# Kernel tuning notes

Measured on AMD Instinct MI355X. Metric: run time of the kernel, lower is better.

Reference implementation:

```python
import jax, jax.numpy as jnp
import numpy as np

B, T, I, H, O = 64, 512, 256, 1024, 10

def setup_inputs() -> dict:
    key = jax.random.key(0)
    ks = jax.random.split(key, 7)
    s_x = 1.0 / np.sqrt(I)
    s_h = 1.0 / np.sqrt(H)
    return {
        "x": jax.random.normal(ks[0], (B, T, I), dtype=jnp.float32),
        "Wx": jax.random.uniform(ks[1], (4, I, H), jnp.float32, -s_x, s_x),
        "bx": jax.random.uniform(ks[2], (4, H), jnp.float32, -s_x, s_x),
        "Wh": jax.random.uniform(ks[3], (4, H, H), jnp.float32, -s_h, s_h),
        "bh": jax.random.uniform(ks[4], (4, H), jnp.float32, -s_h, s_h),
        "Wp": jax.random.uniform(ks[5], (H, O), jnp.float32, -s_h, s_h),
        "bp": jax.random.uniform(ks[6], (O,), jnp.float32, -s_h, s_h),
    }

def reference(x, Wx, bx, Wh, bh, Wp, bp):
    # Gate order along axis 0: g (tanh), i, f, o (sigmoid).
    batch, seq, _ = x.shape
    hid = Wh.shape[-1]
    # Precompute all input-side gate projections: [T, 4, B, H]
    gx_all = jnp.einsum('bti,kih->tkbh', x, Wx) + bx[None, :, None, :]

    def step(carry, gx_t):
        h, c = carry
        z = gx_t + jnp.einsum('bh,kho->kbo', h, Wh) + bh[:, None, :]  # [4,B,H]
        g = jnp.tanh(z[0])
        i = jax.nn.sigmoid(z[1])
        f = jax.nn.sigmoid(z[2])
        o = jax.nn.sigmoid(z[3])
        c = g * i + c * f
        h = jnp.tanh(c) * o
        return (h, c), None

    h0 = jnp.zeros((batch, hid), dtype=x.dtype)
    c0 = jnp.zeros((batch, hid), dtype=x.dtype)
    (h, _), _ = jax.lax.scan(step, (h0, c0), gx_all)
    p = h @ Wp + bp
    return jax.nn.softmax(p, axis=1)
```

## Files before the change

### kernel.cpp

```cpp
#include <hip/hip_runtime.h>
#include <cstdint>
#include <cstddef>

#define B_  64
#define T_  512
#define I_  256
#define H_  1024
#define O_  10
#define ZST 68
#define ZPW (64 * ZST)
#define ZBUF (4 * ZPW)
#define LDS_ALLOC 139264

typedef __attribute__((ext_vector_type(4))) float f32x4;
typedef __attribute__((ext_vector_type(8))) short s16x8;
typedef unsigned long long u64;

__device__ inline unsigned short f2bf(float f) {
    unsigned int u = __float_as_uint(f);
    u += 0x7fffu + ((u >> 16) & 1u);
    return (unsigned short)(u >> 16);
}
__device__ inline float bf2f(unsigned short h) {
    return __uint_as_float(((unsigned int)h) << 16);
}
__device__ inline float fsig(float x)  { return 1.0f / (1.0f + __expf(-x)); }
__device__ inline float ftanh(float x) { return 1.0f - 2.0f / (1.0f + __expf(2.0f * x)); }

#define ALD32(p)    __hip_atomic_load((p), __ATOMIC_RELAXED, __HIP_MEMORY_SCOPE_AGENT)
#define AST32(p, v) __hip_atomic_store((p), (v), __ATOMIC_RELAXED, __HIP_MEMORY_SCOPE_AGENT)
#define ALD64(p)    __hip_atomic_load((p), __ATOMIC_RELAXED, __HIP_MEMORY_SCOPE_AGENT)
#define AST64(p, v) __hip_atomic_store((p), (v), __ATOMIC_RELAXED, __HIP_MEMORY_SCOPE_AGENT)

__global__ __launch_bounds__(256) void cast_xT_kernel(const float* __restrict__ x,
                                                      unsigned short* __restrict__ xb) {
    int idx = blockIdx.x * 256 + threadIdx.x;
    int ic4 = idx & 63, rest = idx >> 6;
    int t = rest & 511, b = rest >> 9;
    float4 v = ((const float4*)x)[((size_t)(b * T_ + t)) * 64 + ic4];
    ((ushort4*)xb)[((size_t)(t * B_ + b)) * 64 + ic4] =
        make_ushort4(f2bf(v.x), f2bf(v.y), f2bf(v.z), f2bf(v.w));
}

__global__ __launch_bounds__(256) void pack_wh_kernel(const float* __restrict__ Wh,
                                                      uint4* __restrict__ whp) {
    int e = blockIdx.x * 256 + threadIdx.x;
    int lane = e & 63, nt = (e >> 6) & 3, kt = (e >> 8) & 31, nb = e >> 13;
    int q = (lane & 15) >> 2, cc = lane & 3;
    int hh = nb * 16 + nt * 4 + cc;
    int k0 = kt * 32 + (lane >> 4) * 8;
    const float* src = Wh + (size_t)q * (H_ * H_) + (size_t)k0 * H_ + hh;
    unsigned short u[8];
#pragma unroll
    for (int j = 0; j < 8; ++j) u[j] = f2bf(src[(size_t)j * H_]);
    uint4 out;
    out.x = (unsigned)u[0] | ((unsigned)u[1] << 16);
    out.y = (unsigned)u[2] | ((unsigned)u[3] << 16);
    out.z = (unsigned)u[4] | ((unsigned)u[5] << 16);
    out.w = (unsigned)u[6] | ((unsigned)u[7] << 16);
    whp[e] = out;
}

__global__ __launch_bounds__(256) void pack_wx_kernel(const float* __restrict__ Wx,
                                                      uint4* __restrict__ wxp) {
    int e = blockIdx.x * 256 + threadIdx.x;
    int lane = e & 63, nt = (e >> 6) & 3, kt = (e >> 8) & 7, nb = e >> 11;
    int q = (lane & 15) >> 2, cc = lane & 3;
    int hh = nb * 16 + nt * 4 + cc;
    int i0 = kt * 32 + (lane >> 4) * 8;
    const float* src = Wx + (size_t)q * (I_ * H_) + (size_t)i0 * H_ + hh;
    unsigned short u[8];
#pragma unroll
    for (int j = 0; j < 8; ++j) u[j] = f2bf(src[(size_t)j * H_]);
    uint4 out;
    out.x = (unsigned)u[0] | ((unsigned)u[1] << 16);
    out.y = (unsigned)u[2] | ((unsigned)u[3] << 16);
    out.z = (unsigned)u[4] | ((unsigned)u[5] << 16);
    out.w = (unsigned)u[6] | ((unsigned)u[7] << 16);
    wxp[e] = out;
}

__global__ __launch_bounds__(256, 1) void lstm_kernel(const unsigned short* __restrict__ xb,
                                                      const uint4* __restrict__ whp,
                                                      const uint4* __restrict__ wxp,
                                                      const float* __restrict__ bx,
                                                      const float* __restrict__ bh,
                                                      const float* __restrict__ Wp,
                                                      const float* __restrict__ bp,
                                                      unsigned short* __restrict__ hbuf,
                                                      unsigned int* __restrict__ flags,
                                                      float* __restrict__ out) {
    extern __shared__ float zpart[];
    int tid = threadIdx.x, lane = tid & 63, w = tid >> 6;
    int nb = blockIdx.x;
    unsigned int* done = flags + 768;

    if (nb >= 64) {
        float a = 1.0f + (float)tid * 0.001f;
        const float bm = 1.0000001f, cm = 0.9999999f;
        while (ALD32(done) == 0u) {
#pragma unroll
            for (int i = 0; i < 512; ++i) a = __builtin_fmaf(a, bm, cm);
        }
        if (__float_as_uint(a) == 0xDEADBEEFu) AST32(&flags[200], 1u);
        return;
    }

    int ma = lane & 15, quad = lane >> 4;

    const s16x8* whpp = (const s16x8*)whp;
    const s16x8* wxpp = (const s16x8*)wxp;
    s16x8 whf[4][8], wxf[4][2];
#pragma unroll
    for (int nt = 0; nt < 4; ++nt) {
#pragma unroll
        for (int k = 0; k < 8; ++k)
            whf[nt][k] = whpp[nb * 8192 + (w * 8 + k) * 256 + nt * 64 + lane];
#pragma unroll
        for (int k = 0; k < 2; ++k)
            wxf[nt][k] = wxpp[nb * 2048 + (w * 2 + k) * 256 + nt * 64 + lane];
    }

    int gb = tid >> 2, wq = tid & 3;
    float bias[4][4];
#pragma unroll
    for (int g = 0; g < 4; ++g)
#pragma unroll
        for (int i = 0; i < 4; ++i) {
            int n = g * H_ + nb * 16 + wq * 4 + i;
            bias[g][i] = bx[n] + bh[n];
        }

    u64* hbase = (u64*)hbuf;

    AST64(&hbase[nb * 256 + tid], 0ull);
    asm volatile("s_waitcnt vmcnt(0)" ::: "memory");
    if (lane == 0) AST32(&flags[nb * 4 + w], 1u);

    float cst[4] = {0.f, 0.f, 0.f, 0.f};

    for (int t = 0; t < T_; ++t) {
        s16x8 Ax[4][2];
#pragma unroll
        for (int mt = 0; mt < 4; ++mt) {
            const unsigned short* xrow =
                xb + ((size_t)t * B_ + mt * 16 + ma) * I_ + w * 64 + quad * 8;
            Ax[mt][0] = *(const s16x8*)xrow;
            Ax[mt][1] = *(const s16x8*)(xrow + 32);
        }

        {
            unsigned tgt = (unsigned)(t + 1);
            for (;;) {
                unsigned v = ALD32(&flags[w * 64 + lane]);
                if (__ballot(v < tgt) == 0ull) break;
                __builtin_amdgcn_s_sleep(1);
            }
        }

        const u64* hp = hbase + (size_t)(t & 3) * 16384;
        u64*       hn = hbase + (size_t)((t + 1) & 3) * 16384;

        u64 Ah[4][16];
#pragma unroll
        for (int mt = 0; mt < 4; ++mt) {
            int row = mt * 16 + ma;
#pragma unroll
            for (int kl = 0; kl < 8; ++kl) {
                const u64* p = hp + ((size_t)((w * 8 + kl) * 2 + (quad >> 1))) * 256
                               + (size_t)row * 4 + (quad & 1) * 2;
                Ah[mt][kl * 2]     = ALD64(p);
                Ah[mt][kl * 2 + 1] = ALD64(p + 1);
            }
        }

        f32x4 acc[4][4] = {};
#pragma unroll
        for (int mt = 0; mt < 4; ++mt) {
#pragma unroll
            for (int kl = 0; kl < 8; ++kl) {
                union { u64 q[2]; s16x8 v; } au;
                au.q[0] = Ah[mt][kl * 2];
                au.q[1] = Ah[mt][kl * 2 + 1];
#pragma unroll
                for (int nt = 0; nt < 4; ++nt)
                    acc[mt][nt] = __builtin_amdgcn_mfma_f32_16x16x32_bf16(au.v, whf[nt][kl],
                                                                          acc[mt][nt], 0, 0, 0);
            }
#pragma unroll
            for (int kx = 0; kx < 2; ++kx)
#pragma unroll
                for (int nt = 0; nt < 4; ++nt)
                    acc[mt][nt] = __builtin_amdgcn_mfma_f32_16x16x32_bf16(Ax[mt][kx], wxf[nt][kx],
                                                                          acc[mt][nt], 0, 0, 0);
        }

        float* zb = zpart + (size_t)(t & 1) * ZBUF;
        float* zp = zb + w * ZPW;
#pragma unroll
        for (int mt = 0; mt < 4; ++mt)
#pragma unroll
            for (int nt = 0; nt < 4; ++nt)
#pragma unroll
                for (int r = 0; r < 4; ++r)
                    zp[(mt * 16 + quad * 4 + r) * ZST + nt * 16 + ma] = acc[mt][nt][r];
        __syncthreads();

        float zs[4][4];
#pragma unroll
        for (int g = 0; g < 4; ++g) {
            float4 s = make_float4(0.f, 0.f, 0.f, 0.f);
#pragma unroll
            for (int p = 0; p < 4; ++p) {
                float4 v = *(const float4*)(zb + p * ZPW + gb * ZST + wq * 16 + g * 4);
                s.x += v.x; s.y += v.y; s.z += v.z; s.w += v.w;
            }
            zs[g][0] = s.x; zs[g][1] = s.y; zs[g][2] = s.z; zs[g][3] = s.w;
        }
        unsigned short hh[4];
#pragma unroll
        for (int i = 0; i < 4; ++i) {
            float g  = ftanh(zs[0][i] + bias[0][i]);
            float ii = fsig (zs[1][i] + bias[1][i]);
            float ff = fsig (zs[2][i] + bias[2][i]);
            float oo = fsig (zs[3][i] + bias[3][i]);
            float c  = g * ii + cst[i] * ff;
            cst[i] = c;
            hh[i] = f2bf(ftanh(c) * oo);
        }
        u64 hv = (u64)hh[0] | ((u64)hh[1] << 16) | ((u64)hh[2] << 32) | ((u64)hh[3] << 48);
        AST64(&hn[nb * 256 + tid], hv);

        asm volatile("s_waitcnt vmcnt(0)" ::: "memory");
        if (lane == 0) AST32(&flags[nb * 4 + w], (unsigned)(t + 2));
    }

    {
        unsigned tgt = (unsigned)(T_ + 1);
        for (;;) {
            unsigned v = ALD32(&flags[w * 64 + lane]);
            if (__ballot(v < tgt) == 0ull) break;
            __builtin_amdgcn_s_sleep(1);
        }
    }
    __syncthreads();
    if (nb == 0 && tid == 0) AST32(done, 1u);

    int b = nb;
    union { u64 q; unsigned short s[4]; } hu;
    hu.q = ALD64(&hbase[(tid >> 2) * 256 + b * 4 + (tid & 3)]);
    int j0 = (tid >> 2) * 16 + (tid & 3) * 4;
    float pacc[O_];
#pragma unroll
    for (int o = 0; o < O_; ++o) pacc[o] = 0.f;
#pragma unroll
    for (int j = 0; j < 4; ++j) {
        float hvv = bf2f(hu.s[j]);
        const float* wr = Wp + (size_t)(j0 + j) * O_;
#pragma unroll
        for (int o = 0; o < O_; ++o) pacc[o] += hvv * wr[o];
    }
    float* red = zpart;
#pragma unroll
    for (int o = 0; o < O_; ++o) red[tid * O_ + o] = pacc[o];
    __syncthreads();
    for (int s2 = 128; s2 > 0; s2 >>= 1) {
        if (tid < s2) {
#pragma unroll
            for (int o = 0; o < O_; ++o) red[tid * O_ + o] += red[(tid + s2) * O_ + o];
        }
        __syncthreads();
    }
    if (tid == 0) {
        float p[O_];
        for (int o = 0; o < O_; ++o) p[o] = red[o] + bp[o];
        float mx = p[0];
        for (int o = 1; o < O_; ++o) mx = fmaxf(mx, p[o]);
        float e[O_], sum = 0.f;
        for (int o = 0; o < O_; ++o) { e[o] = __expf(p[o] - mx); sum += e[o]; }
        float inv = 1.f / sum;
        for (int o = 0; o < O_; ++o) out[b * O_ + o] = e[o] * inv;
    }
}

extern "C" void kernel_launch(void* const* d_in, const int* in_sizes, int n_in,
                              void* d_out, int out_size, void* d_ws, size_t ws_size,
                              hipStream_t stream) {
    (void)in_sizes; (void)n_in; (void)out_size; (void)ws_size;
    const float* x  = (const float*)d_in[0];
    const float* Wx = (const float*)d_in[1];
    const float* bx = (const float*)d_in[2];
    const float* Wh = (const float*)d_in[3];
    const float* bh = (const float*)d_in[4];
    const float* Wp = (const float*)d_in[5];
    const float* bp = (const float*)d_in[6];

    const size_t xbB  = (size_t)T_ * B_ * I_ * 2;
    const size_t whpB = (size_t)4 * H_ * H_ * 2;
    const size_t wxpB = (size_t)4 * I_ * H_ * 2;
    const size_t hB   = (size_t)4 * B_ * H_ * 2;

    char* ws = (char*)d_ws;
    unsigned short* xb    = (unsigned short*)ws;
    uint4*          whp   = (uint4*)(ws + xbB);
    uint4*          wxp   = (uint4*)(ws + xbB + whpB);
    unsigned short* hbuf  = (unsigned short*)(ws + xbB + whpB + wxpB);
    unsigned int*   flags = (unsigned int*)(ws + xbB + whpB + wxpB + hB);

    static bool attr_set = false;
    if (!attr_set) {
        (void)hipFuncSetAttribute((const void*)lstm_kernel,
                                  hipFuncAttributeMaxDynamicSharedMemorySize, LDS_ALLOC);
        attr_set = true;
    }

    hipError_t e0 = hipMemsetAsync(flags, 0, 4096, stream);
    (void)e0;
    cast_xT_kernel<<<8192, 256, 0, stream>>>(x, xb);
    pack_wh_kernel<<<2048, 256, 0, stream>>>(Wh, whp);
    pack_wx_kernel<<< 512, 256, 0, stream>>>(Wx, wxp);
    lstm_kernel<<<64 + 192, 256, LDS_ALLOC, stream>>>(xb, whp, wxp, bx, bh, Wp, bp, hbuf, flags,
                                                      (float*)d_out);
}
```

Measured before the change: 3.990 ms.

## Overlap input-projection MFMAs and next-step x loads with the flag wait

Restructures the persistent LSTM time loop into a two-step unrolled macro with double-buffered x fragments. The x tile for step t+1 is prefetched during step t, and the Wx MFMAs now run before the cross-block flag spin-wait, so they overlap barrier latency. The spin loop drops s_sleep and polls only after an early probe fails. Weight fragments are pinned to AGPRs via inline asm to relieve VGPR pressure. The risks are higher register use or spills, busier polling traffic on the flags, and a fragile dependence on compiler scheduling.

```diff
diff --git a/kernel.cpp b/kernel.cpp
--- a/kernel.cpp
+++ b/kernel.cpp
@@ -31,6 +31,8 @@
 #define AST32(p, v) __hip_atomic_store((p), (v), __ATOMIC_RELAXED, __HIP_MEMORY_SCOPE_AGENT)
 #define ALD64(p)    __hip_atomic_load((p), __ATOMIC_RELAXED, __HIP_MEMORY_SCOPE_AGENT)
 #define AST64(p, v) __hip_atomic_store((p), (v), __ATOMIC_RELAXED, __HIP_MEMORY_SCOPE_AGENT)
+
+#define PIN_A(x) asm volatile("" : "+a"(x))
 
 __global__ __launch_bounds__(256) void cast_xT_kernel(const float* __restrict__ x,
                                                       unsigned short* __restrict__ xb) {
@@ -120,6 +122,13 @@
         for (int k = 0; k < 2; ++k)
             wxf[nt][k] = wxpp[nb * 2048 + (w * 2 + k) * 256 + nt * 64 + lane];
     }
+#pragma unroll
+    for (int nt = 0; nt < 4; ++nt) {
+#pragma unroll
+        for (int k = 0; k < 8; ++k) PIN_A(whf[nt][k]);
+#pragma unroll
+        for (int k = 0; k < 2; ++k) PIN_A(wxf[nt][k]);
+    }
 
     int gb = tid >> 2, wq = tid & 3;
     float bias[4][4];
@@ -139,101 +148,132 @@
 
     float cst[4] = {0.f, 0.f, 0.f, 0.f};
 
-    for (int t = 0; t < T_; ++t) {
-        s16x8 Ax[4][2];
-#pragma unroll
-        for (int mt = 0; mt < 4; ++mt) {
-            const unsigned short* xrow =
-                xb + ((size_t)t * B_ + mt * 16 + ma) * I_ + w * 64 + quad * 8;
-            Ax[mt][0] = *(const s16x8*)xrow;
-            Ax[mt][1] = *(const s16x8*)(xrow + 32);
-        }
-
-        {
-            unsigned tgt = (unsigned)(t + 1);
-            for (;;) {
-                unsigned v = ALD32(&flags[w * 64 + lane]);
-                if (__ballot(v < tgt) == 0ull) break;
-                __builtin_amdgcn_s_sleep(1);
-            }
-        }
-
-        const u64* hp = hbase + (size_t)(t & 3) * 16384;
-        u64*       hn = hbase + (size_t)((t + 1) & 3) * 16384;
-
-        u64 Ah[4][16];
-#pragma unroll
-        for (int mt = 0; mt < 4; ++mt) {
-            int row = mt * 16 + ma;
-#pragma unroll
-            for (int kl = 0; kl < 8; ++kl) {
-                const u64* p = hp + ((size_t)((w * 8 + kl) * 2 + (quad >> 1))) * 256
-                               + (size_t)row * 4 + (quad & 1) * 2;
-                Ah[mt][kl * 2]     = ALD64(p);
-                Ah[mt][kl * 2 + 1] = ALD64(p + 1);
-            }
-        }
-
-        f32x4 acc[4][4] = {};
-#pragma unroll
-        for (int mt = 0; mt < 4; ++mt) {
-#pragma unroll
-            for (int kl = 0; kl < 8; ++kl) {
-                union { u64 q[2]; s16x8 v; } au;
-                au.q[0] = Ah[mt][kl * 2];
-                au.q[1] = Ah[mt][kl * 2 + 1];
-#pragma unroll
-                for (int nt = 0; nt < 4; ++nt)
-                    acc[mt][nt] = __builtin_amdgcn_mfma_f32_16x16x32_bf16(au.v, whf[nt][kl],
-                                                                          acc[mt][nt], 0, 0, 0);
-            }
-#pragma unroll
-            for (int kx = 0; kx < 2; ++kx)
-#pragma unroll
-                for (int nt = 0; nt < 4; ++nt)
-                    acc[mt][nt] = __builtin_amdgcn_mfma_f32_16x16x32_bf16(Ax[mt][kx], wxf[nt][kx],
-                                                                          acc[mt][nt], 0, 0, 0);
-        }
-
-        float* zb = zpart + (size_t)(t & 1) * ZBUF;
-        float* zp = zb + w * ZPW;
-#pragma unroll
-        for (int mt = 0; mt < 4; ++mt)
-#pragma unroll
-            for (int nt = 0; nt < 4; ++nt)
-#pragma unroll
-                for (int r = 0; r < 4; ++r)
-                    zp[(mt * 16 + quad * 4 + r) * ZST + nt * 16 + ma] = acc[mt][nt][r];
-        __syncthreads();
-
-        float zs[4][4];
-#pragma unroll
-        for (int g = 0; g < 4; ++g) {
-            float4 s = make_float4(0.f, 0.f, 0.f, 0.f);
-#pragma unroll
-            for (int p = 0; p < 4; ++p) {
-                float4 v = *(const float4*)(zb + p * ZPW + gb * ZST + wq * 16 + g * 4);
-                s.x += v.x; s.y += v.y; s.z += v.z; s.w += v.w;
-            }
-            zs[g][0] = s.x; zs[g][1] = s.y; zs[g][2] = s.z; zs[g][3] = s.w;
-        }
-        unsigned short hh[4];
-#pragma unroll
-        for (int i = 0; i < 4; ++i) {
-            float g  = ftanh(zs[0][i] + bias[0][i]);
-            float ii = fsig (zs[1][i] + bias[1][i]);
-            float ff = fsig (zs[2][i] + bias[2][i]);
-            float oo = fsig (zs[3][i] + bias[3][i]);
-            float c  = g * ii + cst[i] * ff;
-            cst[i] = c;
-            hh[i] = f2bf(ftanh(c) * oo);
-        }
-        u64 hv = (u64)hh[0] | ((u64)hh[1] << 16) | ((u64)hh[2] << 32) | ((u64)hh[3] << 48);
-        AST64(&hn[nb * 256 + tid], hv);
-
-        asm volatile("s_waitcnt vmcnt(0)" ::: "memory");
-        if (lane == 0) AST32(&flags[nb * 4 + w], (unsigned)(t + 2));
-    }
+    s16x8 AxA[4][2], AxB[4][2];
+#define LOAD_AX(DST, tt)                                                        \
+    {                                                                           \
+        int ts_ = (tt) < T_ ? (tt) : (T_ - 1);                                  \
+        _Pragma("unroll")                                                       \
+        for (int mt = 0; mt < 4; ++mt) {                                        \
+            const unsigned short* xr_ =                                         \
+                xb + ((size_t)ts_ * B_ + mt * 16 + ma) * I_ + w * 64 + quad * 8;\
+            DST[mt][0] = *(const s16x8*)xr_;                                    \
+            DST[mt][1] = *(const s16x8*)(xr_ + 32);                             \
+        }                                                                       \
+    }
+    LOAD_AX(AxA, 0)
+
+#define STEP(t, CUR, NXT)                                                       \
+    {                                                                           \
+                    \
+        unsigned probe = ALD32(&flags[w * 64 + lane]);                          \
+        __builtin_amdgcn_sched_barrier(0);                                      \
+                                                                                \
+               \
+        f32x4 acc[4][4] = {};                                                   \
+        _Pragma("unroll")                                                       \
+        for (int mt = 0; mt < 4; ++mt)                                          \
+            _Pragma("unroll")                                                   \
+            for (int kx = 0; kx < 2; ++kx)                                      \
+                _Pragma("unroll")                                               \
+                for (int nt = 0; nt < 4; ++nt)                                  \
+                    acc[mt][nt] = __builtin_amdgcn_mfma_f32_16x16x32_bf16(      \
+                        CUR[mt][kx], wxf[nt][kx], acc[mt][nt], 0, 0, 0);        \
+        __builtin_amdgcn_sched_barrier(0);                                      \
+                                                                                \
+                  \
+        {                                                                       \
+            unsigned tgt = (unsigned)((t) + 1);                                 \
+            if (__ballot(probe < tgt) != 0ull) {                                \
+                for (;;) {                                                      \
+                    unsigned v = ALD32(&flags[w * 64 + lane]);                  \
+                    if (__ballot(v < tgt) == 0ull) break;                       \
+                }                                                               \
+            }                                                                   \
+        }                                                                       \
+                                                                                \
+        const u64* hp = hbase + (size_t)((t) & 3) * 16384;                      \
+        u64*       hn = hbase + (size_t)(((t) + 1) & 3) * 16384;                \
+                                                                                \
+                         \
+        u64 Ah[4][16];                                                          \
+        _Pragma("unroll")                                                       \
+        for (int mt = 0; mt < 4; ++mt) {                                        \
+            int row = mt * 16 + ma;                                             \
+            _Pragma("unroll")                                                   \
+            for (int kl = 0; kl < 8; ++kl) {                                    \
+                const u64* p = hp + ((size_t)((w * 8 + kl) * 2 + (quad >> 1))) * 256 \
+                               + (size_t)row * 4 + (quad & 1) * 2;              \
+                Ah[mt][kl * 2]     = ALD64(p);                                  \
+                Ah[mt][kl * 2 + 1] = ALD64(p + 1);                              \
+            }                                                                   \
+        }                                                                       \
+                                                                                \
+        _Pragma("unroll")                                                       \
+        for (int mt = 0; mt < 4; ++mt) {                                        \
+            _Pragma("unroll")                                                   \
+            for (int kl = 0; kl < 8; ++kl) {                                    \
+                union { u64 q[2]; s16x8 v; } au;                                \
+                au.q[0] = Ah[mt][kl * 2];                                       \
+                au.q[1] = Ah[mt][kl * 2 + 1];                                   \
+                _Pragma("unroll")                                               \
+                for (int nt = 0; nt < 4; ++nt)                                  \
+                    acc[mt][nt] = __builtin_amdgcn_mfma_f32_16x16x32_bf16(      \
+                        au.v, whf[nt][kl], acc[mt][nt], 0, 0, 0);               \
+            }                                                                   \
+        }                                                                       \
+                                                                                \
+            \
+        LOAD_AX(NXT, (t) + 1)                                                   \
+                                                                                \
+                \
+        float* zb = zpart + (size_t)((t) & 1) * ZBUF;                           \
+        float* zp = zb + w * ZPW;                                               \
+        _Pragma("unroll")                                                       \
+        for (int mt = 0; mt < 4; ++mt)                                          \
+            _Pragma("unroll")                                                   \
+            for (int nt = 0; nt < 4; ++nt)                                      \
+                _Pragma("unroll")                                               \
+                for (int r = 0; r < 4; ++r)                                     \
+                    zp[(mt * 16 + quad * 4 + r) * ZST + nt * 16 + ma] = acc[mt][nt][r]; \
+        __syncthreads();                                                        \
+                                                                                \
+                            \
+        float zs[4][4];                                                         \
+        _Pragma("unroll")                                                       \
+        for (int g = 0; g < 4; ++g) {                                           \
+            float4 s = make_float4(0.f, 0.f, 0.f, 0.f);                         \
+            _Pragma("unroll")                                                   \
+            for (int p = 0; p < 4; ++p) {                                       \
+                float4 v = *(const float4*)(zb + p * ZPW + gb * ZST + wq * 16 + g * 4); \
+                s.x += v.x; s.y += v.y; s.z += v.z; s.w += v.w;                 \
+            }                                                                   \
+            zs[g][0] = s.x; zs[g][1] = s.y; zs[g][2] = s.z; zs[g][3] = s.w;     \
+        }                                                                       \
+        unsigned short hh[4];                                                   \
+        _Pragma("unroll")                                                       \
+        for (int i = 0; i < 4; ++i) {                                           \
+            float g  = ftanh(zs[0][i] + bias[0][i]);                            \
+            float ii = fsig (zs[1][i] + bias[1][i]);                            \
+            float ff = fsig (zs[2][i] + bias[2][i]);                            \
+            float oo = fsig (zs[3][i] + bias[3][i]);                            \
+            float c  = g * ii + cst[i] * ff;                                    \
+            cst[i] = c;                                                         \
+            hh[i] = f2bf(ftanh(c) * oo);                                        \
+        }                                                                       \
+        u64 hv = (u64)hh[0] | ((u64)hh[1] << 16) | ((u64)hh[2] << 32) | ((u64)hh[3] << 48); \
+        AST64(&hn[nb * 256 + tid], hv);                                         \
+                                                                                \
+                          \
+        asm volatile("s_waitcnt vmcnt(0)" ::: "memory");                        \
+        if (lane == 0) AST32(&flags[nb * 4 + w], (unsigned)((t) + 2));          \
+    }
+
+    for (int t2 = 0; t2 < T_; t2 += 2) {
+        STEP(t2,     AxA, AxB)
+        STEP(t2 + 1, AxB, AxA)
+    }
+#undef STEP
+#undef LOAD_AX
 
     {
         unsigned tgt = (unsigned)(T_ + 1);
```

Result: slower. 4.539 ms (+13.7%).
